# Performance work log

Measured on AMD Instinct MI355X. Metric: run time of the kernel, lower is better.

## Reference

```python
import jax, jax.numpy as jnp
import numpy as np

N = 100000       # nodes
E = 1200000      # edges
D_IN = 64
D_OUT = 64
ALPHA = 0.01     # LeakyReLU negative slope
EPS = 1e-5       # BatchNorm eps


def setup_inputs() -> dict:
    key = jax.random.key(0)
    k0, k1, k2, k3 = jax.random.split(key, 4)
    x = jax.random.normal(k0, (N, D_IN), dtype=jnp.float32)
    edge_idx = jax.random.randint(k1, (2, E), 0, N)
    edge_attr = jax.random.uniform(k2, (E,), dtype=jnp.float32)
    W = jax.random.normal(k3, (D_IN, D_OUT), dtype=jnp.float32) * (1.0 / np.sqrt(D_IN))
    b = jnp.zeros((D_OUT,), dtype=jnp.float32)
    gamma = jnp.ones((D_OUT,), dtype=jnp.float32)
    beta = jnp.zeros((D_OUT,), dtype=jnp.float32)
    return {"x": x, "edge_idx": edge_idx, "edge_attr": edge_attr,
            "W": W, "b": b, "gamma": gamma, "beta": beta}


def reference(x, edge_idx, edge_attr, W, b, gamma, beta):
    n = x.shape[0]
    row, col = edge_idx[0], edge_idx[1]
    # --- GCNConv: add self-loops, symmetric normalization ---
    loops = jnp.arange(n)
    row_f = jnp.concatenate([row, loops])                       # [E+N]
    col_f = jnp.concatenate([col, loops])                       # [E+N]
    w_f = jnp.concatenate([edge_attr, jnp.ones((n,), x.dtype)])  # [E+N]
    deg = jax.ops.segment_sum(w_f, col_f, num_segments=n)       # [N]
    deg_safe = jnp.where(deg > 0, deg, 1.0)
    dis = jnp.where(deg > 0, jax.lax.rsqrt(deg_safe), 0.0)      # deg^-1/2
    norm = dis[row_f] * w_f * dis[col_f]                        # [E+N]
    h = x @ W                                                   # [N, D_OUT]
    msg = norm[:, None] * h[row_f]                              # gather + scale
    agg = jax.ops.segment_sum(msg, col_f, num_segments=n) + b   # scatter-add
    # --- BatchNorm (training-mode batch stats, biased var) ---
    mean = jnp.mean(agg, axis=0)
    var = jnp.mean((agg - mean) ** 2, axis=0)
    hn = (agg - mean) * jax.lax.rsqrt(var + EPS) * gamma + beta
    # --- LeakyReLU ---
    return jnp.where(hn >= 0, hn, ALPHA * hn)
```

## Files before the change

kernel.cpp:

```cpp
#include <hip/hip_runtime.h>

#define D 64
#define ALPHA 0.01f
#define EPS 1e-5f
#define NREP 8
#define CAP 48
#define GSZ 128
#define GMAX 1024
#define NB 256

typedef __attribute__((ext_vector_type(8))) short short8;
typedef __attribute__((ext_vector_type(4))) float f32x4;

__device__ inline unsigned short f2bf(float f) {
    unsigned u = __float_as_uint(f);
    u += 0x7fffu + ((u >> 16) & 1u);
    return (unsigned short)(u >> 16);
}
__device__ inline float bf2f(unsigned short h) { return __uint_as_float((unsigned)h << 16); }

__global__ void k_prep(const float4* __restrict__ x4, ushort4* __restrict__ xb4,
                       float* __restrict__ stats, long long n16) {
    long long i = (long long)blockIdx.x * blockDim.x + threadIdx.x;
    if (i < n16) {
        float4 v = x4[i];
        ushort4 r;
        r.x = f2bf(v.x); r.y = f2bf(v.y); r.z = f2bf(v.z); r.w = f2bf(v.w);
        xb4[i] = r;
    }
    if (i < NREP * 128) stats[i] = 0.0f;
}

__global__ __launch_bounds__(256) void k_binA(const int* __restrict__ col,
                                              int* __restrict__ cnt_gb, int G, int E) {
    __shared__ int h[GMAX];
    int b = blockIdx.x;
    for (int i = threadIdx.x; i < G; i += 256) h[i] = 0;
    __syncthreads();
    int chunk = (E + NB - 1) / NB;
    int e0 = b * chunk;
    int e1 = e0 + chunk; if (e1 > E) e1 = E;
    for (int e = e0 + threadIdx.x; e < e1; e += 256)
        atomicAdd(&h[col[e] >> 7], 1);
    __syncthreads();
    for (int i = threadIdx.x; i < G; i += 256)
        cnt_gb[i * NB + b] = h[i];
}

__global__ __launch_bounds__(256) void k_scanA(const int* __restrict__ cnt_gb,
                                               int* __restrict__ bsum, int M) {
    __shared__ int ls[256];
    int base = blockIdx.x * 1024 + threadIdx.x * 4;
    int s = 0;
    if (base + 3 < M) {
        int4 v = *(const int4*)&cnt_gb[base];
        s = v.x + v.y + v.z + v.w;
    } else {
#pragma unroll
        for (int k = 0; k < 4; ++k) { int idx = base + k; if (idx < M) s += cnt_gb[idx]; }
    }
    ls[threadIdx.x] = s;
    __syncthreads();
    for (int off = 128; off > 0; off >>= 1) {
        if (threadIdx.x < off) ls[threadIdx.x] += ls[threadIdx.x + off];
        __syncthreads();
    }
    if (threadIdx.x == 0) bsum[blockIdx.x] = ls[0];
}

__global__ __launch_bounds__(256) void k_scanC(const int* __restrict__ cnt_gb,
                                               const int* __restrict__ bsum,
                                               int* __restrict__ pos,
                                               int* __restrict__ gseg, int M, int G, int E) {
    __shared__ int ls[256];
    int t = threadIdx.x;
    ls[t] = (t < blockIdx.x) ? bsum[t] : 0;
    __syncthreads();
    for (int off = 128; off > 0; off >>= 1) {
        if (t < off) ls[t] += ls[t + off];
        __syncthreads();
    }
    int base_total = ls[0];
    __syncthreads();
    int base = blockIdx.x * 1024 + t * 4;
    int v[4];
    int s = 0;
#pragma unroll
    for (int k = 0; k < 4; ++k) { int idx = base + k; v[k] = (idx < M) ? cnt_gb[idx] : 0; s += v[k]; }
    ls[t] = s;
    __syncthreads();
    int own = s;
    for (int off = 1; off < 256; off <<= 1) {
        int tv = (t >= off) ? ls[t - off] : 0;
        __syncthreads();
        ls[t] += tv;
        __syncthreads();
    }
    int excl = ls[t] - own + base_total;
#pragma unroll
    for (int k = 0; k < 4; ++k) {
        int idx = base + k;
        if (idx < M) {
            pos[idx] = excl;
            if ((idx & (NB - 1)) == 0) gseg[idx >> 8] = excl;
        }
        excl += v[k];
    }
    if (blockIdx.x == 0 && t == 0) gseg[G] = E;
}

__global__ __launch_bounds__(256) void k_binB(const int* __restrict__ eidx,
                                              const float* __restrict__ w,
                                              const int* __restrict__ pos,
                                              uint2* __restrict__ seg, int G, int E) {
    __shared__ int cursor[GMAX];
    int b = blockIdx.x;
    for (int g = threadIdx.x; g < G; g += 256) cursor[g] = pos[g * NB + b];
    __syncthreads();
    int chunk = (E + NB - 1) / NB;
    int e0 = b * chunk;
    int e1 = e0 + chunk; if (e1 > E) e1 = E;
    for (int e = e0 + threadIdx.x; e < e1; e += 256) {
        int row = eidx[e];
        int c = eidx[E + e];
        unsigned wq = (unsigned)(w[e] * 32767.0f + 0.5f);
        int slot = atomicAdd(&cursor[c >> 7], 1);
        seg[slot] = make_uint2((wq << 17) | (unsigned)row, (unsigned)(c & (GSZ - 1)));
    }
}

__global__ __launch_bounds__(256) void k_binC(const uint2* __restrict__ seg,
                                              const int* __restrict__ gseg,
                                              unsigned* __restrict__ bucket,
                                              int* __restrict__ cnt,
                                              float* __restrict__ dis, int n) {
    __shared__ int cl[GSZ];
    __shared__ float ws[GSZ];
    int g = blockIdx.x;
    if (threadIdx.x < GSZ) { cl[threadIdx.x] = 0; ws[threadIdx.x] = 0.0f; }
    __syncthreads();
    int s0 = gseg[g], s1 = gseg[g + 1];
    for (int i = s0 + threadIdx.x; i < s1; i += 256) {
        uint2 ev = seg[i];
        int cig = (int)ev.y;
        int rank = atomicAdd(&cl[cig], 1);
        atomicAdd(&ws[cig], (float)(ev.x >> 17) * (1.0f / 32767.0f));
        int node = g * GSZ + cig;
        if (rank < CAP) bucket[(size_t)node * CAP + rank] = ev.x;
    }
    __syncthreads();
    if (threadIdx.x < GSZ) {
        int node = g * GSZ + threadIdx.x;
        if (node < n) {
            cnt[node] = cl[threadIdx.x];
            dis[node] = rsqrtf(1.0f + ws[threadIdx.x]);
        }
    }
}

__global__ __launch_bounds__(256) void k_gather(const unsigned short* __restrict__ xb,
                                                const unsigned* __restrict__ bucket,
                                                const int* __restrict__ cnt,
                                                const float* __restrict__ dis,
                                                unsigned short* __restrict__ aggb, int n) {
    int node = blockIdx.x * 4 + (threadIdx.x >> 6);
    if (node >= n) return;
    int lane = threadIdx.x & 63;
    int g = lane >> 3;
    int l = lane & 7;
    int c = cnt[node];
    if (c > CAP) c = CAP;
    float di = dis[node];
    float acc[8] = {0, 0, 0, 0, 0, 0, 0, 0};
    if (g == 0) {
        float sl = di * di;
        short8 xv = *(const short8*)(xb + (size_t)node * 64 + l * 8);
#pragma unroll
        for (int k = 0; k < 8; ++k) acc[k] = bf2f((unsigned short)xv[k]) * sl;
    }
    for (int j = g; j < c; j += 8) {
        unsigned v = bucket[(size_t)node * CAP + j];
        int src = (int)(v & 0x1FFFFu);
        float we = (float)(v >> 17) * (1.0f / 32767.0f);
        float nrm = we * dis[src] * di;
        short8 xv = *(const short8*)(xb + (size_t)src * 64 + l * 8);
#pragma unroll
        for (int k = 0; k < 8; ++k) acc[k] += nrm * bf2f((unsigned short)xv[k]);
    }
#pragma unroll
    for (int off = 8; off <= 32; off <<= 1)
#pragma unroll
        for (int k = 0; k < 8; ++k) acc[k] += __shfl_xor(acc[k], off, 64);
    if (g == 0) {
        short8 r;
#pragma unroll
        for (int k = 0; k < 8; ++k) r[k] = (short)f2bf(acc[k]);
        *(short8*)(aggb + (size_t)node * 64 + l * 8) = r;
    }
}

__global__ __launch_bounds__(256) void k_gemmstats(const unsigned short* __restrict__ aggb,
                                                   const float* __restrict__ Wm,
                                                   float* __restrict__ out,
                                                   float* __restrict__ stats, int n) {
    __shared__ unsigned short Wt[64 * 64];
    __shared__ float ssum[4][64], qsum[4][64];
    int tid = threadIdx.x;
    for (int i = tid; i < 4096; i += 256) {
        int k = i >> 6, nn = i & 63;
        Wt[nn * 64 + k] = f2bf(Wm[i]);
    }
    __syncthreads();
    int wv = tid >> 6;
    int lane = tid & 63;
    int l15 = lane & 15;
    int quad = lane >> 4;

    short8 bfrag[2][4];
#pragma unroll
    for (int h = 0; h < 2; ++h)
#pragma unroll
        for (int g = 0; g < 4; ++g)
            bfrag[h][g] = *(const short8*)&Wt[(g * 16 + l15) * 64 + h * 32 + quad * 8];

    float s[4] = {0, 0, 0, 0}, q[4] = {0, 0, 0, 0};
    int nwt = (n + 15) >> 4;
    for (int wt = blockIdx.x * 4 + wv; wt < nwt; wt += gridDim.x * 4) {
        int row0 = wt * 16;
        int arow = row0 + l15;
        if (arow >= n) arow = n - 1;
        const unsigned short* ap = aggb + (size_t)arow * 64 + quad * 8;
        short8 a0 = *(const short8*)ap;
        short8 a1 = *(const short8*)(ap + 32);
        f32x4 acc[4] = {{0, 0, 0, 0}, {0, 0, 0, 0}, {0, 0, 0, 0}, {0, 0, 0, 0}};
#pragma unroll
        for (int g = 0; g < 4; ++g) {
            acc[g] = __builtin_amdgcn_mfma_f32_16x16x32_bf16(a0, bfrag[0][g], acc[g], 0, 0, 0);
            acc[g] = __builtin_amdgcn_mfma_f32_16x16x32_bf16(a1, bfrag[1][g], acc[g], 0, 0, 0);
        }
#pragma unroll
        for (int r = 0; r < 4; ++r) {
            int row = row0 + quad * 4 + r;
            if (row < n) {
                size_t base = (size_t)row * 64;
#pragma unroll
                for (int g = 0; g < 4; ++g) {
                    float v = acc[g][r];
                    out[base + g * 16 + l15] = v;
                    s[g] += v;
                    q[g] += v * v;
                }
            }
        }
    }
#pragma unroll
    for (int off = 16; off <= 32; off <<= 1) {
#pragma unroll
        for (int g = 0; g < 4; ++g) {
            s[g] += __shfl_xor(s[g], off, 64);
            q[g] += __shfl_xor(q[g], off, 64);
        }
    }
    if (quad == 0) {
#pragma unroll
        for (int g = 0; g < 4; ++g) { ssum[wv][g * 16 + l15] = s[g]; qsum[wv][g * 16 + l15] = q[g]; }
    }
    __syncthreads();
    float* st = stats + (blockIdx.x & (NREP - 1)) * 128;
    if (tid < 64)
        atomicAdd(&st[tid], ssum[0][tid] + ssum[1][tid] + ssum[2][tid] + ssum[3][tid]);
    else if (tid < 128) {
        int t = tid - 64;
        atomicAdd(&st[64 + t], qsum[0][t] + qsum[1][t] + qsum[2][t] + qsum[3][t]);
    }
}

__global__ __launch_bounds__(256) void k_norm(float4* __restrict__ out4,
                                              const float* __restrict__ stats,
                                              const float* __restrict__ gamma,
                                              const float* __restrict__ beta, int n) {
    __shared__ float scale[64], shift[64];
    if (threadIdx.x < 64) {
        float sm = 0.0f, qm = 0.0f;
#pragma unroll
        for (int r = 0; r < NREP; ++r) {
            sm += stats[r * 128 + threadIdx.x];
            qm += stats[r * 128 + 64 + threadIdx.x];
        }
        float inv_n = 1.0f / (float)n;
        float mean = sm * inv_n;
        float var = qm * inv_n - mean * mean;
        float sc = rsqrtf(var + EPS) * gamma[threadIdx.x];
        scale[threadIdx.x] = sc;
        shift[threadIdx.x] = beta[threadIdx.x] - mean * sc;
    }
    __syncthreads();
    long long idx = (long long)blockIdx.x * blockDim.x + threadIdx.x;
    if (idx < (long long)n * 16) {
        int l = (int)(idx & 15);
        float4 v = out4[idx];
        float4 r;
        float a, b2;
        a = scale[l * 4 + 0]; b2 = shift[l * 4 + 0]; r.x = v.x * a + b2; r.x = r.x >= 0.0f ? r.x : ALPHA * r.x;
        a = scale[l * 4 + 1]; b2 = shift[l * 4 + 1]; r.y = v.y * a + b2; r.y = r.y >= 0.0f ? r.y : ALPHA * r.y;
        a = scale[l * 4 + 2]; b2 = shift[l * 4 + 2]; r.z = v.z * a + b2; r.z = r.z >= 0.0f ? r.z : ALPHA * r.z;
        a = scale[l * 4 + 3]; b2 = shift[l * 4 + 3]; r.w = v.w * a + b2; r.w = r.w >= 0.0f ? r.w : ALPHA * r.w;
        out4[idx] = r;
    }
}

extern "C" void kernel_launch(void* const* d_in, const int* in_sizes, int n_in,
                              void* d_out, int out_size, void* d_ws, size_t ws_size,
                              hipStream_t stream) {
    const float* x     = (const float*)d_in[0];
    const int*   eidx  = (const int*)d_in[1];
    const float* eattr = (const float*)d_in[2];
    const float* Wm    = (const float*)d_in[3];
    const float* gamma = (const float*)d_in[5];
    const float* beta  = (const float*)d_in[6];
    float* out = (float*)d_out;

    int n = in_sizes[0] / D;
    int E = in_sizes[2];
    int G = (n + GSZ - 1) / GSZ;
    int M = G * NB;
    int nbs = (M + 1023) / 1024;

    char* p = (char*)d_ws;
    uint2* seg = (uint2*)p;                     p += (size_t)E * 8;
    unsigned* bucket = (unsigned*)p;            p += (size_t)n * CAP * 4;
    unsigned short* xb   = (unsigned short*)p;  p += (size_t)n * D * 2;
    unsigned short* aggb = (unsigned short*)p;  p += (size_t)n * D * 2;
    int* cnt = (int*)p;                         p += (size_t)n * 4;
    float* dis = (float*)p;                     p += (size_t)n * 4;
    float* stats = (float*)p;                   p += NREP * 128 * 4;
    int* cnt_gb = (int*)p;                      p += (size_t)M * 4;
    int* pos = (int*)p;                         p += (size_t)M * 4;
    int* gseg = (int*)p;                        p += ((size_t)G + 1) * 4;
    int* bsum = (int*)p;                        p += 256 * 4;

    long long n16 = (long long)n * 16;

    k_prep<<<(unsigned)((n16 + 255) / 256), 256, 0, stream>>>(
        (const float4*)x, (ushort4*)xb, stats, n16);
    k_binA<<<NB, 256, 0, stream>>>(eidx + E, cnt_gb, G, E);
    k_scanA<<<nbs, 256, 0, stream>>>(cnt_gb, bsum, M);
    k_scanC<<<nbs, 256, 0, stream>>>(cnt_gb, bsum, pos, gseg, M, G, E);
    k_binB<<<NB, 256, 0, stream>>>(eidx, eattr, pos, seg, G, E);
    k_binC<<<G, 256, 0, stream>>>(seg, gseg, bucket, cnt, dis, n);
    k_gather<<<(n + 3) / 4, 256, 0, stream>>>(xb, bucket, cnt, dis, aggb, n);
    k_gemmstats<<<512, 256, 0, stream>>>(aggb, Wm, out, stats, n);
    k_norm<<<(unsigned)((n16 + 255) / 256), 256, 0, stream>>>(
        (float4*)out, stats, gamma, beta, n);
}
```

Before: 194.7 us.

## Merge prep and binning kernels, pipeline gather loads, prescale dis, widen gemm grid

Merges the bf16 conversion kernel and the column-histogram kernel into one launch, using block-index ranges to split the work. The gather loop now processes two bucket entries per iteration and prefetches the next pair of indices. It uses a prescaled dis_s array, so the per-edge multiply by dis[dst] is applied once at the end. The gemm+stats grid is doubled. The trade-off is more register pressure and an extra per-node array written and read.

```diff
diff --git a/kernel.cpp b/kernel.cpp
--- a/kernel.cpp
+++ b/kernel.cpp
@@ -19,32 +19,35 @@
 }
 __device__ inline float bf2f(unsigned short h) { return __uint_as_float((unsigned)h << 16); }
 
-__global__ void k_prep(const float4* __restrict__ x4, ushort4* __restrict__ xb4,
-                       float* __restrict__ stats, long long n16) {
-    long long i = (long long)blockIdx.x * blockDim.x + threadIdx.x;
-    if (i < n16) {
-        float4 v = x4[i];
-        ushort4 r;
-        r.x = f2bf(v.x); r.y = f2bf(v.y); r.z = f2bf(v.z); r.w = f2bf(v.w);
-        xb4[i] = r;
-    }
-    if (i < NREP * 128) stats[i] = 0.0f;
-}
-
-__global__ __launch_bounds__(256) void k_binA(const int* __restrict__ col,
-                                              int* __restrict__ cnt_gb, int G, int E) {
+__global__ __launch_bounds__(256) void k_prepA(const float4* __restrict__ x4,
+                                               ushort4* __restrict__ xb4,
+                                               float* __restrict__ stats,
+                                               const int* __restrict__ col,
+                                               int* __restrict__ cnt_gb,
+                                               long long n16, int G, int E) {
     __shared__ int h[GMAX];
-    int b = blockIdx.x;
-    for (int i = threadIdx.x; i < G; i += 256) h[i] = 0;
-    __syncthreads();
-    int chunk = (E + NB - 1) / NB;
-    int e0 = b * chunk;
-    int e1 = e0 + chunk; if (e1 > E) e1 = E;
-    for (int e = e0 + threadIdx.x; e < e1; e += 256)
-        atomicAdd(&h[col[e] >> 7], 1);
-    __syncthreads();
-    for (int i = threadIdx.x; i < G; i += 256)
-        cnt_gb[i * NB + b] = h[i];
+    if (blockIdx.x < NB) {
+        int b = blockIdx.x;
+        for (int i = threadIdx.x; i < G; i += 256) h[i] = 0;
+        __syncthreads();
+        int chunk = (E + NB - 1) / NB;
+        int e0 = b * chunk;
+        int e1 = e0 + chunk; if (e1 > E) e1 = E;
+        for (int e = e0 + threadIdx.x; e < e1; e += 256)
+            atomicAdd(&h[col[e] >> 7], 1);
+        __syncthreads();
+        for (int i = threadIdx.x; i < G; i += 256)
+            cnt_gb[i * NB + b] = h[i];
+    } else {
+        long long i = (long long)(blockIdx.x - NB) * 256 + threadIdx.x;
+        if (i < n16) {
+            float4 v = x4[i];
+            ushort4 r;
+            r.x = f2bf(v.x); r.y = f2bf(v.y); r.z = f2bf(v.z); r.w = f2bf(v.w);
+            xb4[i] = r;
+        }
+        if (i < NREP * 128) stats[i] = 0.0f;
+    }
 }
 
 __global__ __launch_bounds__(256) void k_scanA(const int* __restrict__ cnt_gb,
@@ -133,7 +136,8 @@
                                               const int* __restrict__ gseg,
                                               unsigned* __restrict__ bucket,
                                               int* __restrict__ cnt,
-                                              float* __restrict__ dis, int n) {
+                                              float* __restrict__ dis,
+                                              float* __restrict__ dis_s, int n) {
     __shared__ int cl[GSZ];
     __shared__ float ws[GSZ];
     int g = blockIdx.x;
@@ -153,7 +157,9 @@
         int node = g * GSZ + threadIdx.x;
         if (node < n) {
             cnt[node] = cl[threadIdx.x];
-            dis[node] = rsqrtf(1.0f + ws[threadIdx.x]);
+            float d = rsqrtf(1.0f + ws[threadIdx.x]);
+            dis[node] = d;
+            dis_s[node] = d * (1.0f / 32767.0f);
         }
     }
 }
@@ -162,6 +168,7 @@
                                                 const unsigned* __restrict__ bucket,
                                                 const int* __restrict__ cnt,
                                                 const float* __restrict__ dis,
+                                                const float* __restrict__ dis_s,
                                                 unsigned short* __restrict__ aggb, int n) {
     int node = blockIdx.x * 4 + (threadIdx.x >> 6);
     if (node >= n) return;
@@ -173,19 +180,29 @@
     float di = dis[node];
     float acc[8] = {0, 0, 0, 0, 0, 0, 0, 0};
     if (g == 0) {
-        float sl = di * di;
-        short8 xv = *(const short8*)(xb + (size_t)node * 64 + l * 8);
-#pragma unroll
-        for (int k = 0; k < 8; ++k) acc[k] = bf2f((unsigned short)xv[k]) * sl;
-    }
-    for (int j = g; j < c; j += 8) {
-        unsigned v = bucket[(size_t)node * CAP + j];
-        int src = (int)(v & 0x1FFFFu);
-        float we = (float)(v >> 17) * (1.0f / 32767.0f);
-        float nrm = we * dis[src] * di;
-        short8 xv = *(const short8*)(xb + (size_t)src * 64 + l * 8);
-#pragma unroll
-        for (int k = 0; k < 8; ++k) acc[k] += nrm * bf2f((unsigned short)xv[k]);
+        short8 xv = *(const short8*)(xb + ((size_t)node << 6) + l * 8);
+#pragma unroll
+        for (int k = 0; k < 8; ++k) acc[k] = bf2f((unsigned short)xv[k]) * di;
+    }
+    const unsigned* bkt = bucket + (size_t)node * CAP;
+    int j0 = g, j1 = g + 8;
+    unsigned v0 = (j0 < c) ? bkt[j0] : 0u;
+    unsigned v1 = (j1 < c) ? bkt[j1] : 0u;
+    while (j0 < c) {
+        int p0 = j0 + 16, p1 = j1 + 16;
+        unsigned w0 = (p0 < c) ? bkt[p0] : 0u;
+        unsigned w1 = (p1 < c) ? bkt[p1] : 0u;
+        int s0 = (int)(v0 & 0x1FFFFu);
+        int s1 = (int)(v1 & 0x1FFFFu);
+        float nr0 = (float)(v0 >> 17) * dis_s[s0];
+        float nr1 = (float)(v1 >> 17) * dis_s[s1];
+        short8 x0 = *(const short8*)(xb + ((size_t)s0 << 6) + l * 8);
+        short8 x1 = *(const short8*)(xb + ((size_t)s1 << 6) + l * 8);
+#pragma unroll
+        for (int k = 0; k < 8; ++k) acc[k] += nr0 * bf2f((unsigned short)x0[k]);
+#pragma unroll
+        for (int k = 0; k < 8; ++k) acc[k] += nr1 * bf2f((unsigned short)x1[k]);
+        v0 = w0; v1 = w1; j0 = p0; j1 = p1;
     }
 #pragma unroll
     for (int off = 8; off <= 32; off <<= 1)
@@ -194,8 +211,8 @@
     if (g == 0) {
         short8 r;
 #pragma unroll
-        for (int k = 0; k < 8; ++k) r[k] = (short)f2bf(acc[k]);
-        *(short8*)(aggb + (size_t)node * 64 + l * 8) = r;
+        for (int k = 0; k < 8; ++k) r[k] = (short)f2bf(acc[k] * di);
+        *(short8*)(aggb + ((size_t)node << 6) + l * 8) = r;
     }
 }
 
@@ -333,6 +350,7 @@
     unsigned short* aggb = (unsigned short*)p;  p += (size_t)n * D * 2;
     int* cnt = (int*)p;                         p += (size_t)n * 4;
     float* dis = (float*)p;                     p += (size_t)n * 4;
+    float* dis_s = (float*)p;                   p += (size_t)n * 4;
     float* stats = (float*)p;                   p += NREP * 128 * 4;
     int* cnt_gb = (int*)p;                      p += (size_t)M * 4;
     int* pos = (int*)p;                         p += (size_t)M * 4;
@@ -340,16 +358,16 @@
     int* bsum = (int*)p;                        p += 256 * 4;
 
     long long n16 = (long long)n * 16;
-
-    k_prep<<<(unsigned)((n16 + 255) / 256), 256, 0, stream>>>(
-        (const float4*)x, (ushort4*)xb, stats, n16);
-    k_binA<<<NB, 256, 0, stream>>>(eidx + E, cnt_gb, G, E);
+    unsigned prep_blocks = (unsigned)((n16 + 255) / 256);
+
+    k_prepA<<<NB + prep_blocks, 256, 0, stream>>>(
+        (const float4*)x, (ushort4*)xb, stats, eidx + E, cnt_gb, n16, G, E);
     k_scanA<<<nbs, 256, 0, stream>>>(cnt_gb, bsum, M);
     k_scanC<<<nbs, 256, 0, stream>>>(cnt_gb, bsum, pos, gseg, M, G, E);
     k_binB<<<NB, 256, 0, stream>>>(eidx, eattr, pos, seg, G, E);
-    k_binC<<<G, 256, 0, stream>>>(seg, gseg, bucket, cnt, dis, n);
-    k_gather<<<(n + 3) / 4, 256, 0, stream>>>(xb, bucket, cnt, dis, aggb, n);
-    k_gemmstats<<<512, 256, 0, stream>>>(aggb, Wm, out, stats, n);
+    k_binC<<<G, 256, 0, stream>>>(seg, gseg, bucket, cnt, dis, dis_s, n);
+    k_gather<<<(n + 3) / 4, 256, 0, stream>>>(xb, bucket, cnt, dis, dis_s, aggb, n);
+    k_gemmstats<<<1024, 256, 0, stream>>>(aggb, Wm, out, stats, n);
     k_norm<<<(unsigned)((n16 + 255) / 256), 256, 0, stream>>>(
         (float4*)out, stats, gamma, beta, n);
 }
```

After: 185.6 us. -4.6%, faster.
